# Performance work log

Measured on AMD Instinct MI355X. Metric: run time of the kernel, lower is better.

## Reference

```python
import jax, jax.numpy as jnp
import numpy as np
from math import log

MODEL_DIM = 512
NUM_HEADS = 8
DIM_HEAD = 64
INNER = NUM_HEADS * DIM_HEAD
B, L = 8, 1024
EPS = 1e-5


def setup_inputs() -> dict:
    key = jax.random.key(0)
    ks = jax.random.split(key, 9)
    x = jax.random.normal(ks[0], (B, L, MODEL_DIM), dtype=jnp.float32)
    gamma = jnp.ones((MODEL_DIM,), jnp.float32)
    beta = jnp.zeros((MODEL_DIM,), jnp.float32)
    w_qkv = jax.random.normal(ks[1], (3 * INNER, MODEL_DIM), jnp.float32) * (MODEL_DIM ** -0.5)
    b_qkv = jnp.zeros((3 * INNER,), jnp.float32)
    w_pos = jax.random.normal(ks[2], (INNER, MODEL_DIM), jnp.float32) * (MODEL_DIM ** -0.5)
    w_out = jax.random.normal(ks[3], (MODEL_DIM, INNER), jnp.float32) * (INNER ** -0.5)
    b_out = jnp.zeros((MODEL_DIM,), jnp.float32)
    # xavier_uniform for (num_heads, dim_head)
    bound = (6.0 / (NUM_HEADS + DIM_HEAD)) ** 0.5
    u_bias = jax.random.uniform(ks[4], (NUM_HEADS, DIM_HEAD), jnp.float32, -bound, bound)
    v_bias = jax.random.uniform(ks[5], (NUM_HEADS, DIM_HEAD), jnp.float32, -bound, bound)
    return {"x": x, "gamma": gamma, "beta": beta, "w_qkv": w_qkv, "b_qkv": b_qkv,
            "w_pos": w_pos, "w_out": w_out, "b_out": b_out, "u_bias": u_bias, "v_bias": v_bias}


def _rel_pos_emb(seq_len, d):
    # (L, D): (i - j) scaled by sinusoid frequencies, then cos on even cols, sin on odd cols
    rel = (jnp.arange(seq_len, dtype=jnp.float32)[:, None]
           - jnp.arange(d, dtype=jnp.float32)[None, :])
    freqs = jnp.exp(-jnp.arange(0, 2 * d, 2, dtype=jnp.float32) * (log(10000.0) / MODEL_DIM))
    angle = rel * freqs[None, :]
    even = (jnp.arange(d) % 2) == 0
    return jnp.where(even[None, :], jnp.cos(angle), jnp.sin(angle))  # (L, D)


def reference(x, gamma, beta, w_qkv, b_qkv, w_pos, w_out, b_out, u_bias, v_bias):
    b, l, d = x.shape
    h, dh = NUM_HEADS, DIM_HEAD
    # LayerNorm
    mu = jnp.mean(x, axis=-1, keepdims=True)
    var = jnp.mean(jnp.square(x - mu), axis=-1, keepdims=True)
    xn = (x - mu) * jax.lax.rsqrt(var + EPS) * gamma + beta
    # relative position embedding, identical per batch element
    pe = _rel_pos_emb(l, d)                      # (L, D)
    pos = (pe @ w_pos.T).reshape(l, h, dh)       # (L, H, Dh)
    pos = jnp.transpose(pos, (1, 0, 2))          # (H, L, Dh)
    # qkv
    qkv = xn @ w_qkv.T + b_qkv                   # (B, L, 3*inner)
    q, k, v = jnp.split(qkv, 3, axis=-1)
    def to_heads(t):
        return jnp.transpose(t.reshape(b, l, h, dh), (0, 2, 1, 3))  # (B,H,L,Dh)
    q, k, v = to_heads(q), to_heads(k), to_heads(v)
    scale = dh ** -0.5
    content = jnp.einsum('bhld,bhmd->bhlm', q + u_bias[None, :, None, :], k)
    pos_score = jnp.einsum('bhld,hmd->bhlm', q + v_bias[None, :, None, :], pos)
    attn = jax.nn.softmax((content + pos_score) * scale, axis=-1)
    out = jnp.einsum('bhlm,bhmd->bhld', attn, v)
    out = jnp.transpose(out, (0, 2, 1, 3)).reshape(b, l, h * dh)
    return out @ w_out.T + b_out  # dropout p=0.0 -> identity
```

## Files before the change

kernel.cpp:

```cpp
#include <hip/hip_runtime.h>
#include <math.h>

static constexpr int Bn = 8, Ln = 1024, Dm = 512, Hn = 8, DhN = 64;

typedef short bf16x8 __attribute__((ext_vector_type(8)));
typedef float f32x4 __attribute__((ext_vector_type(4)));
typedef _Float16 f16x4 __attribute__((ext_vector_type(4)));
typedef _Float16 f16x8 __attribute__((ext_vector_type(8)));
typedef unsigned int u32x4 __attribute__((ext_vector_type(4)));

#define QSCALE 0.1803368801111137f

static __device__ __forceinline__ unsigned short f2b(float f) {
  union { float f; unsigned int u; } x;
  x.f = f;
  unsigned int u = x.u;
  unsigned int r = (u + 0x7FFFu + ((u >> 16) & 1u)) >> 16;
  return (unsigned short)r;
}
static __device__ __forceinline__ float b2f(unsigned short u) {
  union { unsigned int u; float f; } x;
  x.u = ((unsigned int)u) << 16;
  return x.f;
}

#define GLDS16(g, l)                                                        \
  __builtin_amdgcn_global_load_lds((const __attribute__((address_space(1))) void*)(g), \
                                   (__attribute__((address_space(3))) void*)(l), 16, 0, 0)

__global__ __launch_bounds__(256) void prep1(const float* __restrict__ x,
                                             const float* __restrict__ gamma,
                                             const float* __restrict__ beta,
                                             unsigned short* __restrict__ xn,
                                             unsigned short* __restrict__ pe,
                                             const float* __restrict__ wq, unsigned short* __restrict__ wqb,
                                             const float* __restrict__ wp, unsigned short* __restrict__ wpb,
                                             const float* __restrict__ wo, unsigned short* __restrict__ wob) {
  int b = blockIdx.x;
  int t = threadIdx.x;
  if (b < 8192) {
    const float2 v = *(const float2*)(x + (size_t)b * Dm + t * 2);
    float s = v.x + v.y;
    float sq = v.x * v.x + v.y * v.y;
#pragma unroll
    for (int off = 32; off > 0; off >>= 1) {
      s += __shfl_down(s, off);
      sq += __shfl_down(sq, off);
    }
    __shared__ float red[8];
    int wave = t >> 6, lane = t & 63;
    if (lane == 0) { red[wave * 2] = s; red[wave * 2 + 1] = sq; }
    __syncthreads();
    float S = red[0] + red[2] + red[4] + red[6];
    float SQ = red[1] + red[3] + red[5] + red[7];
    float mu = S * (1.0f / Dm);
    float var = SQ * (1.0f / Dm) - mu * mu;
    float rstd = rsqrtf(var + 1e-5f);
    int c = t * 2;
    ushort2 o;
    o.x = f2b((v.x - mu) * rstd * gamma[c] + beta[c]);
    o.y = f2b((v.y - mu) * rstd * gamma[c + 1] + beta[c + 1]);
    *(ushort2*)(xn + (size_t)b * Dm + c) = o;
  } else if (b < 10240) {
    int idx = (b - 8192) * 256 + t;
    int l = idx >> 9, k = idx & 511;
    float freq = expf(-0.0359778921f * (float)k);
    float angle = (float)(l - k) * freq;
    pe[idx] = f2b((k & 1) ? sinf(angle) : cosf(angle));
  } else {
    int cb = b - 10240;
    const float* src;
    unsigned short* dst;
    int off;
    if (cb < 768) { src = wq; dst = wqb; off = cb; }
    else if (cb < 1024) { src = wp; dst = wpb; off = cb - 768; }
    else { src = wo; dst = wob; off = cb - 1024; }
    int i = off * 256 + t;
    float4 v = *(const float4*)(src + (size_t)i * 4);
    ushort4 o;
    o.x = f2b(v.x); o.y = f2b(v.y); o.z = f2b(v.z); o.w = f2b(v.w);
    *(ushort4*)(dst + (size_t)i * 4) = o;
  }
}

__global__ __launch_bounds__(256, 8) void gemm_mfma(const unsigned short* __restrict__ Ain,
                                                    const unsigned short* __restrict__ Bwin,
                                                    const float* __restrict__ biasin,
                                                    float* __restrict__ outfin,
                                                    unsigned short* __restrict__ oq,
                                                    unsigned short* __restrict__ ok,
                                                    unsigned short* __restrict__ ov,
                                                    const unsigned short* __restrict__ A2,
                                                    const unsigned short* __restrict__ B2,
                                                    float* __restrict__ outf2,
                                                    int K, int mode) {
  int by = blockIdx.y, bx = blockIdx.x;
  const unsigned short* A = Ain;
  const unsigned short* Bw = Bwin;
  const float* bias = biasin;
  float* outf = outfin;
  if (by >= 128) {
    if (bx >= 8) return;
    A = A2; Bw = B2; bias = nullptr; outf = outf2; mode = 1; by -= 128;
  }
  __shared__ alignas(16) unsigned short As[64 * 64];
  __shared__ alignas(16) unsigned short Bs[64 * 64];
  const int t = threadIdx.x;
  const int lane = t & 63, w = t >> 6;
  const int c = lane & 15, q8 = lane >> 4;
  const int wm = (w & 1) * 32, wn = (w >> 1) * 32;
  const int m0 = by * 64, n0 = bx * 64;

  f32x4 acc[2][2];
#pragma unroll
  for (int i = 0; i < 2; ++i)
#pragma unroll
    for (int j = 0; j < 2; ++j) acc[i][j] = (f32x4){0.f, 0.f, 0.f, 0.f};

  const int srow = lane >> 3;
  const int sgr = (lane & 7) ^ srow;

  for (int k0 = 0; k0 < K; k0 += 64) {
    __syncthreads();
#pragma unroll
    for (int j = 0; j < 2; ++j) {
      int r = j * 32 + w * 8 + srow;
      GLDS16(A + (size_t)(m0 + r) * K + k0 + sgr * 8, As + (j * 256 + w * 64 + lane) * 8);
      GLDS16(Bw + (size_t)(n0 + r) * K + k0 + sgr * 8, Bs + (j * 256 + w * 64 + lane) * 8);
    }
    __syncthreads();
#pragma unroll
    for (int kk = 0; kk < 2; ++kk) {
      bf16x8 a[2], b[2];
      const int q = kk * 4 + q8;
#pragma unroll
      for (int i = 0; i < 2; ++i) {
        int r = wm + i * 16 + c;
        a[i] = *(const bf16x8*)&As[(r * 8 + (q ^ (r & 7))) * 8];
      }
#pragma unroll
      for (int j = 0; j < 2; ++j) {
        int r = wn + j * 16 + c;
        b[j] = *(const bf16x8*)&Bs[(r * 8 + (q ^ (r & 7))) * 8];
      }
#pragma unroll
      for (int i = 0; i < 2; ++i)
#pragma unroll
        for (int j = 0; j < 2; ++j)
          acc[i][j] = __builtin_amdgcn_mfma_f32_16x16x32_bf16(a[i], b[j], acc[i][j], 0, 0, 0);
    }
  }
#pragma unroll
  for (int i = 0; i < 2; ++i) {
#pragma unroll
    for (int r = 0; r < 4; ++r) {
      int m = m0 + wm + i * 16 + q8 * 4 + r;
#pragma unroll
      for (int j = 0; j < 2; ++j) {
        int n = n0 + wn + j * 16 + c;
        float val = acc[i][j][r] + (bias ? bias[n] : 0.0f);
        if (mode == 0) {
          int part = n >> 9, h = (n >> 6) & 7, dh = n & 63;
          int bb = m >> 10, l = m & 1023;
          size_t idx = (size_t)((bb * 8 + h) * 1024 + l) * 64 + dh;
          if (part == 0) {
            oq[idx] = f2b(val * QSCALE);
          } else if (part == 1) {
            ok[idx] = f2b(val);
          } else {
            union { _Float16 h; unsigned short u; } cv;
            cv.h = (_Float16)val;
            ov[idx] = cv.u;
          }
        } else if (mode == 1) {
          int h = n >> 6, dh = n & 63;
          outf[(size_t)(h * 1024 + m) * 64 + dh] = val;
        } else {
          outf[(size_t)m * 512 + n] = val;
        }
      }
    }
  }
}

__global__ __launch_bounds__(256) void prep2(unsigned short* __restrict__ kbuf,
                                             const float* __restrict__ pos,
                                             const float* __restrict__ ub,
                                             const float* __restrict__ vbb,
                                             float* __restrict__ biasout,
                                             const unsigned short* __restrict__ v,
                                             unsigned short* __restrict__ vt) {
  int b = blockIdx.x;
  int t = threadIdx.x;
  if (b < 16384) {
    int wave = t >> 6, lane = t & 63;
    int g = b * 4 + wave;
    int h = (g >> 10) & 7;
    int m = g & 1023;
    float kv = b2f(kbuf[(size_t)g * 64 + lane]);
    float pv = pos[(size_t)(h * 1024 + m) * 64 + lane];
    float val = ub[h * 64 + lane] * kv + vbb[h * 64 + lane] * pv;
#pragma unroll
    for (int off = 32; off > 0; off >>= 1) val += __shfl_down(val, off);
    if (lane == 0) biasout[g] = val * QSCALE;
    kbuf[(size_t)g * 64 + lane] = f2b(kv + pv);
  } else {
    __shared__ unsigned short Ts[64 * 68];
    int bb = b - 16384;
    int bh = bb >> 4, lt = bb & 15;
    const unsigned short* vg = v + (size_t)bh * 65536 + lt * 4096;
#pragma unroll
    for (int s = 0; s < 4; ++s) {
      int idx = t + s * 256;
      int r = idx >> 4, c4 = (idx & 15) << 2;
      *(ushort4*)&Ts[r * 68 + c4] = *(const ushort4*)(vg + r * 64 + c4);
    }
    __syncthreads();
#pragma unroll
    for (int s = 0; s < 4; ++s) {
      int idx = t + s * 256;
      int d = idx >> 4, l4 = (idx & 15) << 2;
      ushort4 o;
      o.x = Ts[(l4 + 0) * 68 + d];
      o.y = Ts[(l4 + 1) * 68 + d];
      o.z = Ts[(l4 + 2) * 68 + d];
      o.w = Ts[(l4 + 3) * 68 + d];
      int pb = ((l4 >> 2) & 3) * 16 + ((l4 >> 4) & 3) * 4;
      *(ushort4*)(vt + (size_t)bh * 65536 + d * 1024 + lt * 64 + pb) = o;
    }
  }
}

__global__ __launch_bounds__(512) void flash_mfma(const unsigned short* __restrict__ qbf,
                                                  const unsigned short* __restrict__ kbf,
                                                  const unsigned short* __restrict__ vt,
                                                  const float* __restrict__ bias,
                                                  unsigned short* __restrict__ attn_out) {
  __shared__ alignas(16) unsigned short Ks[2][64 * 64];
  __shared__ alignas(16) unsigned short Vs[2][64 * 64];
  __shared__ alignas(16) float Bls[1024];
  const int t = threadIdx.x;
  const int lane = t & 63, w = t >> 6;
  const int c = lane & 15, q8 = lane >> 4;
  const int cc7 = c & 7;
  const int bh = blockIdx.y, qt = blockIdx.x;
  const unsigned short* qg = qbf + (size_t)bh * 65536;
  const unsigned short* kg = kbf + (size_t)bh * 65536;
  const unsigned short* vg = vt + (size_t)bh * 65536;
  const float* bg = bias + (size_t)bh * 1024;

  if (t < 256) GLDS16(bg + t * 4, Bls + t * 4);

  const int ql = qt * 128 + w * 16 + c;
  const bf16x8 bq0 = *(const bf16x8*)(qg + (size_t)ql * 64 + q8 * 8);
  const bf16x8 bq1 = *(const bf16x8*)(qg + (size_t)ql * 64 + 32 + q8 * 8);

  float m_st = -INFINITY, l_st = 0.0f;
  f32x4 o[4];
#pragma unroll
  for (int i = 0; i < 4; ++i) o[i] = (f32x4){0.f, 0.f, 0.f, 0.f};

  const int srow = lane >> 3;
  const int sgr = (lane & 7) ^ srow;
  const int r0 = w * 8 + srow;

  u32x4 pk[2], pv[2];
#pragma unroll
  for (int h = 0; h < 2; ++h) {
    pk[h] = *(const u32x4*)(kg + (size_t)(h * 64 + r0) * 64 + sgr * 8);
    pv[h] = *(const u32x4*)(vg + (size_t)r0 * 1024 + h * 64 + sgr * 8);
  }

  for (int it = 0; it < 8; ++it) {
    __syncthreads();
#pragma unroll
    for (int h = 0; h < 2; ++h) {
      *(u32x4*)&Ks[h][(r0 * 8 + (lane & 7)) * 8] = pk[h];
      *(u32x4*)&Vs[h][(r0 * 8 + (lane & 7)) * 8] = pv[h];
    }
    __syncthreads();
    if (it < 7) {
#pragma unroll
      for (int h = 0; h < 2; ++h) {
        pk[h] = *(const u32x4*)(kg + (size_t)((it + 1) * 128 + h * 64 + r0) * 64 + sgr * 8);
        pv[h] = *(const u32x4*)(vg + (size_t)r0 * 1024 + (it + 1) * 128 + h * 64 + sgr * 8);
      }
    }

    f32x4 sc[2][4];
#pragma unroll
    for (int h = 0; h < 2; ++h) {
#pragma unroll
      for (int nt = 0; nt < 4; ++nt) {
        f32x4 ci = *(const f32x4*)&Bls[it * 128 + h * 64 + nt * 16 + q8 * 4];
        const int row = nt * 16 + c;
        bf16x8 ak0 = *(const bf16x8*)&Ks[h][(row * 8 + (q8 ^ cc7)) * 8];
        bf16x8 ak1 = *(const bf16x8*)&Ks[h][(row * 8 + ((q8 + 4) ^ cc7)) * 8];
        ci = __builtin_amdgcn_mfma_f32_16x16x32_bf16(ak0, bq0, ci, 0, 0, 0);
        sc[h][nt] = __builtin_amdgcn_mfma_f32_16x16x32_bf16(ak1, bq1, ci, 0, 0, 0);
      }
    }
    float mx = sc[0][0][0];
#pragma unroll
    for (int h = 0; h < 2; ++h)
#pragma unroll
      for (int nt = 0; nt < 4; ++nt)
#pragma unroll
        for (int r = 0; r < 4; ++r) mx = fmaxf(mx, sc[h][nt][r]);
    mx = fmaxf(mx, __shfl_xor(mx, 16));
    mx = fmaxf(mx, __shfl_xor(mx, 32));
    float mn = fmaxf(m_st, mx);
    float al = __builtin_amdgcn_exp2f(m_st - mn);
    float su = 0.0f;
    f16x4 pf[2][4];
#pragma unroll
    for (int h = 0; h < 2; ++h)
#pragma unroll
      for (int nt = 0; nt < 4; ++nt)
#pragma unroll
        for (int r = 0; r < 4; ++r) {
          float p = __builtin_amdgcn_exp2f(sc[h][nt][r] - mn);
          su += p;
          pf[h][nt][r] = (_Float16)p;
        }
    su += __shfl_xor(su, 16);
    su += __shfl_xor(su, 32);
    l_st = l_st * al + su;
    m_st = mn;
#pragma unroll
    for (int i = 0; i < 4; ++i) o[i] *= al;
#pragma unroll
    for (int i = 0; i < 4; ++i) {
      const int row = i * 16 + c;
#pragma unroll
      for (int h = 0; h < 2; ++h) {
        f16x8 v01 = *(const f16x8*)&Vs[h][(row * 8 + ((2 * q8) ^ cc7)) * 8];
        f16x8 v23 = *(const f16x8*)&Vs[h][(row * 8 + ((2 * q8 + 1) ^ cc7)) * 8];
        f16x4 a0 = {v01[0], v01[1], v01[2], v01[3]};
        f16x4 a1 = {v01[4], v01[5], v01[6], v01[7]};
        f16x4 a2 = {v23[0], v23[1], v23[2], v23[3]};
        f16x4 a3 = {v23[4], v23[5], v23[6], v23[7]};
        o[i] = __builtin_amdgcn_mfma_f32_16x16x16f16(a0, pf[h][0], o[i], 0, 0, 0);
        o[i] = __builtin_amdgcn_mfma_f32_16x16x16f16(a1, pf[h][1], o[i], 0, 0, 0);
        o[i] = __builtin_amdgcn_mfma_f32_16x16x16f16(a2, pf[h][2], o[i], 0, 0, 0);
        o[i] = __builtin_amdgcn_mfma_f32_16x16x16f16(a3, pf[h][3], o[i], 0, 0, 0);
      }
    }
  }
  const int bidx = bh >> 3, h = bh & 7;
  float inv = 1.0f / l_st;
  size_t base = (size_t)(bidx * 1024 + ql) * 512 + h * 64;
#pragma unroll
  for (int i = 0; i < 4; ++i) {
    ushort4 ov4;
    ov4.x = f2b(o[i][0] * inv);
    ov4.y = f2b(o[i][1] * inv);
    ov4.z = f2b(o[i][2] * inv);
    ov4.w = f2b(o[i][3] * inv);
    *(ushort4*)(attn_out + base + i * 16 + q8 * 4) = ov4;
  }
}

extern "C" void kernel_launch(void* const* d_in, const int* in_sizes, int n_in,
                              void* d_out, int out_size, void* d_ws, size_t ws_size,
                              hipStream_t stream) {
  const float* x      = (const float*)d_in[0];
  const float* gamma  = (const float*)d_in[1];
  const float* beta   = (const float*)d_in[2];
  const float* w_qkv  = (const float*)d_in[3];
  const float* b_qkv  = (const float*)d_in[4];
  const float* w_pos  = (const float*)d_in[5];
  const float* w_out  = (const float*)d_in[6];
  const float* b_out  = (const float*)d_in[7];
  const float* u_bias = (const float*)d_in[8];
  const float* v_bias = (const float*)d_in[9];
  float* out = (float*)d_out;

  unsigned short* wsu = (unsigned short*)d_ws;
  unsigned short* xnb   = wsu;
  unsigned short* peb   = wsu + 4194304;
  unsigned short* wqkvb = wsu + 4718592;
  unsigned short* wposb = wsu + 5505024;
  unsigned short* woutb = wsu + 5767168;
  unsigned short* qbf   = wsu + 6291456;
  unsigned short* kbf   = wsu + 10485760;
  unsigned short* vbf   = wsu + 14680064;
  unsigned short* vtb   = wsu + 18874368;
  unsigned short* attnb = wsu + 23068672;
  float* posb  = (float*)(wsu + 27262976);
  float* biasb = (float*)(wsu + 28311552);

  prep1<<<11520, 256, 0, stream>>>(x, gamma, beta, xnb, peb,
                                   w_qkv, wqkvb, w_pos, wposb, w_out, woutb);
  gemm_mfma<<<dim3(24, 144), 256, 0, stream>>>(xnb, wqkvb, b_qkv, nullptr, qbf, kbf, vbf,
                                               peb, wposb, posb, 512, 0);
  prep2<<<17408, 256, 0, stream>>>(kbf, posb, u_bias, v_bias, biasb, vbf, vtb);
  flash_mfma<<<dim3(8, 64), 512, 0, stream>>>(qbf, kbf, vtb, biasb, attnb);
  gemm_mfma<<<dim3(8, 128), 256, 0, stream>>>(attnb, woutb, b_out, out, nullptr, nullptr, nullptr,
                                              nullptr, nullptr, nullptr, 512, 2);
}
```

Baseline: 177.8 us.

## Process two query tiles per wave in flash attention with 256-thread blocks

The flash attention kernel now runs 4 waves per block instead of 8, and each wave handles two 16-row query groups. Each K/V fragment read from shared memory therefore feeds twice as many MFMAs, and each thread loads twice as many K/V rows into LDS. The aim is to cut LDS read traffic and barrier cost per unit of work. In exchange, register pressure roughly doubles for accumulators and scores, and each block has fewer waves for latency hiding, partly offset by launch_bounds(256,2).

New measurement: 176.8 us. No clear change (-0.6%).

```diff
diff --git a/kernel.cpp b/kernel.cpp
--- a/kernel.cpp
+++ b/kernel.cpp
@@ -231,11 +231,11 @@
   }
 }
 
-__global__ __launch_bounds__(512) void flash_mfma(const unsigned short* __restrict__ qbf,
-                                                  const unsigned short* __restrict__ kbf,
-                                                  const unsigned short* __restrict__ vt,
-                                                  const float* __restrict__ bias,
-                                                  unsigned short* __restrict__ attn_out) {
+__global__ __launch_bounds__(256, 2) void flash_mfma(const unsigned short* __restrict__ qbf,
+                                                     const unsigned short* __restrict__ kbf,
+                                                     const unsigned short* __restrict__ vt,
+                                                     const float* __restrict__ bias,
+                                                     unsigned short* __restrict__ attn_out) {
   __shared__ alignas(16) unsigned short Ks[2][64 * 64];
   __shared__ alignas(16) unsigned short Vs[2][64 * 64];
   __shared__ alignas(16) float Bls[1024];
@@ -249,45 +249,60 @@
   const unsigned short* vg = vt + (size_t)bh * 65536;
   const float* bg = bias + (size_t)bh * 1024;
 
-  if (t < 256) GLDS16(bg + t * 4, Bls + t * 4);
-
-  const int ql = qt * 128 + w * 16 + c;
-  const bf16x8 bq0 = *(const bf16x8*)(qg + (size_t)ql * 64 + q8 * 8);
-  const bf16x8 bq1 = *(const bf16x8*)(qg + (size_t)ql * 64 + 32 + q8 * 8);
-
-  float m_st = -INFINITY, l_st = 0.0f;
-  f32x4 o[4];
-#pragma unroll
-  for (int i = 0; i < 4; ++i) o[i] = (f32x4){0.f, 0.f, 0.f, 0.f};
+  GLDS16(bg + t * 4, Bls + t * 4);
+
+  bf16x8 bq[2][2];
+#pragma unroll
+  for (int g = 0; g < 2; ++g) {
+    int qlg = qt * 128 + g * 64 + w * 16 + c;
+    bq[g][0] = *(const bf16x8*)(qg + (size_t)qlg * 64 + q8 * 8);
+    bq[g][1] = *(const bf16x8*)(qg + (size_t)qlg * 64 + 32 + q8 * 8);
+  }
+
+  float m_st[2] = {-INFINITY, -INFINITY}, l_st[2] = {0.0f, 0.0f};
+  f32x4 o[2][4];
+#pragma unroll
+  for (int g = 0; g < 2; ++g)
+#pragma unroll
+    for (int i = 0; i < 4; ++i) o[g][i] = (f32x4){0.f, 0.f, 0.f, 0.f};
 
   const int srow = lane >> 3;
   const int sgr = (lane & 7) ^ srow;
-  const int r0 = w * 8 + srow;
-
-  u32x4 pk[2], pv[2];
-#pragma unroll
-  for (int h = 0; h < 2; ++h) {
-    pk[h] = *(const u32x4*)(kg + (size_t)(h * 64 + r0) * 64 + sgr * 8);
-    pv[h] = *(const u32x4*)(vg + (size_t)r0 * 1024 + h * 64 + sgr * 8);
-  }
+  const int r0 = w * 16 + srow;
+
+  u32x4 pk[2][2], pv[2][2];
+#pragma unroll
+  for (int h = 0; h < 2; ++h)
+#pragma unroll
+    for (int j = 0; j < 2; ++j) {
+      int r = r0 + j * 8;
+      pk[h][j] = *(const u32x4*)(kg + (size_t)(h * 64 + r) * 64 + sgr * 8);
+      pv[h][j] = *(const u32x4*)(vg + (size_t)r * 1024 + h * 64 + sgr * 8);
+    }
 
   for (int it = 0; it < 8; ++it) {
     __syncthreads();
 #pragma unroll
-    for (int h = 0; h < 2; ++h) {
-      *(u32x4*)&Ks[h][(r0 * 8 + (lane & 7)) * 8] = pk[h];
-      *(u32x4*)&Vs[h][(r0 * 8 + (lane & 7)) * 8] = pv[h];
-    }
+    for (int h = 0; h < 2; ++h)
+#pragma unroll
+      for (int j = 0; j < 2; ++j) {
+        int r = r0 + j * 8;
+        *(u32x4*)&Ks[h][(r * 8 + (lane & 7)) * 8] = pk[h][j];
+        *(u32x4*)&Vs[h][(r * 8 + (lane & 7)) * 8] = pv[h][j];
+      }
     __syncthreads();
     if (it < 7) {
 #pragma unroll
-      for (int h = 0; h < 2; ++h) {
-        pk[h] = *(const u32x4*)(kg + (size_t)((it + 1) * 128 + h * 64 + r0) * 64 + sgr * 8);
-        pv[h] = *(const u32x4*)(vg + (size_t)r0 * 1024 + (it + 1) * 128 + h * 64 + sgr * 8);
-      }
-    }
-
-    f32x4 sc[2][4];
+      for (int h = 0; h < 2; ++h)
+#pragma unroll
+        for (int j = 0; j < 2; ++j) {
+          int r = r0 + j * 8;
+          pk[h][j] = *(const u32x4*)(kg + (size_t)((it + 1) * 128 + h * 64 + r) * 64 + sgr * 8);
+          pv[h][j] = *(const u32x4*)(vg + (size_t)r * 1024 + (it + 1) * 128 + h * 64 + sgr * 8);
+        }
+    }
+
+    f32x4 sc[2][2][4];
 #pragma unroll
     for (int h = 0; h < 2; ++h) {
 #pragma unroll
@@ -296,39 +311,45 @@
         const int row = nt * 16 + c;
         bf16x8 ak0 = *(const bf16x8*)&Ks[h][(row * 8 + (q8 ^ cc7)) * 8];
         bf16x8 ak1 = *(const bf16x8*)&Ks[h][(row * 8 + ((q8 + 4) ^ cc7)) * 8];
-        ci = __builtin_amdgcn_mfma_f32_16x16x32_bf16(ak0, bq0, ci, 0, 0, 0);
-        sc[h][nt] = __builtin_amdgcn_mfma_f32_16x16x32_bf16(ak1, bq1, ci, 0, 0, 0);
-      }
-    }
-    float mx = sc[0][0][0];
-#pragma unroll
-    for (int h = 0; h < 2; ++h)
-#pragma unroll
-      for (int nt = 0; nt < 4; ++nt)
-#pragma unroll
-        for (int r = 0; r < 4; ++r) mx = fmaxf(mx, sc[h][nt][r]);
-    mx = fmaxf(mx, __shfl_xor(mx, 16));
-    mx = fmaxf(mx, __shfl_xor(mx, 32));
-    float mn = fmaxf(m_st, mx);
-    float al = __builtin_amdgcn_exp2f(m_st - mn);
-    float su = 0.0f;
-    f16x4 pf[2][4];
-#pragma unroll
-    for (int h = 0; h < 2; ++h)
-#pragma unroll
-      for (int nt = 0; nt < 4; ++nt)
-#pragma unroll
-        for (int r = 0; r < 4; ++r) {
-          float p = __builtin_amdgcn_exp2f(sc[h][nt][r] - mn);
-          su += p;
-          pf[h][nt][r] = (_Float16)p;
+#pragma unroll
+        for (int g = 0; g < 2; ++g) {
+          f32x4 z = __builtin_amdgcn_mfma_f32_16x16x32_bf16(ak0, bq[g][0], ci, 0, 0, 0);
+          sc[g][h][nt] = __builtin_amdgcn_mfma_f32_16x16x32_bf16(ak1, bq[g][1], z, 0, 0, 0);
         }
-    su += __shfl_xor(su, 16);
-    su += __shfl_xor(su, 32);
-    l_st = l_st * al + su;
-    m_st = mn;
-#pragma unroll
-    for (int i = 0; i < 4; ++i) o[i] *= al;
+      }
+    }
+    f16x4 pf[2][2][4];
+#pragma unroll
+    for (int g = 0; g < 2; ++g) {
+      float mx = sc[g][0][0][0];
+#pragma unroll
+      for (int h = 0; h < 2; ++h)
+#pragma unroll
+        for (int nt = 0; nt < 4; ++nt)
+#pragma unroll
+          for (int r = 0; r < 4; ++r) mx = fmaxf(mx, sc[g][h][nt][r]);
+      mx = fmaxf(mx, __shfl_xor(mx, 16));
+      mx = fmaxf(mx, __shfl_xor(mx, 32));
+      float mn = fmaxf(m_st[g], mx);
+      float al = __builtin_amdgcn_exp2f(m_st[g] - mn);
+      float su = 0.0f;
+#pragma unroll
+      for (int h = 0; h < 2; ++h)
+#pragma unroll
+        for (int nt = 0; nt < 4; ++nt)
+#pragma unroll
+          for (int r = 0; r < 4; ++r) {
+            float p = __builtin_amdgcn_exp2f(sc[g][h][nt][r] - mn);
+            su += p;
+            pf[g][h][nt][r] = (_Float16)p;
+          }
+      su += __shfl_xor(su, 16);
+      su += __shfl_xor(su, 32);
+      l_st[g] = l_st[g] * al + su;
+      m_st[g] = mn;
+#pragma unroll
+      for (int i = 0; i < 4; ++i) o[g][i] *= al;
+    }
 #pragma unroll
     for (int i = 0; i < 4; ++i) {
       const int row = i * 16 + c;
@@ -340,24 +361,31 @@
         f16x4 a1 = {v01[4], v01[5], v01[6], v01[7]};
         f16x4 a2 = {v23[0], v23[1], v23[2], v23[3]};
         f16x4 a3 = {v23[4], v23[5], v23[6], v23[7]};
-        o[i] = __builtin_amdgcn_mfma_f32_16x16x16f16(a0, pf[h][0], o[i], 0, 0, 0);
-        o[i] = __builtin_amdgcn_mfma_f32_16x16x16f16(a1, pf[h][1], o[i], 0, 0, 0);
-        o[i] = __builtin_amdgcn_mfma_f32_16x16x16f16(a2, pf[h][2], o[i], 0, 0, 0);
-        o[i] = __builtin_amdgcn_mfma_f32_16x16x16f16(a3, pf[h][3], o[i], 0, 0, 0);
+#pragma unroll
+        for (int g = 0; g < 2; ++g) {
+          o[g][i] = __builtin_amdgcn_mfma_f32_16x16x16f16(a0, pf[g][h][0], o[g][i], 0, 0, 0);
+          o[g][i] = __builtin_amdgcn_mfma_f32_16x16x16f16(a1, pf[g][h][1], o[g][i], 0, 0, 0);
+          o[g][i] = __builtin_amdgcn_mfma_f32_16x16x16f16(a2, pf[g][h][2], o[g][i], 0, 0, 0);
+          o[g][i] = __builtin_amdgcn_mfma_f32_16x16x16f16(a3, pf[g][h][3], o[g][i], 0, 0, 0);
+        }
       }
     }
   }
   const int bidx = bh >> 3, h = bh & 7;
-  float inv = 1.0f / l_st;
-  size_t base = (size_t)(bidx * 1024 + ql) * 512 + h * 64;
-#pragma unroll
-  for (int i = 0; i < 4; ++i) {
-    ushort4 ov4;
-    ov4.x = f2b(o[i][0] * inv);
-    ov4.y = f2b(o[i][1] * inv);
-    ov4.z = f2b(o[i][2] * inv);
-    ov4.w = f2b(o[i][3] * inv);
-    *(ushort4*)(attn_out + base + i * 16 + q8 * 4) = ov4;
+#pragma unroll
+  for (int g = 0; g < 2; ++g) {
+    int qlg = qt * 128 + g * 64 + w * 16 + c;
+    float inv = 1.0f / l_st[g];
+    size_t base = (size_t)(bidx * 1024 + qlg) * 512 + h * 64;
+#pragma unroll
+    for (int i = 0; i < 4; ++i) {
+      ushort4 ov4;
+      ov4.x = f2b(o[g][i][0] * inv);
+      ov4.y = f2b(o[g][i][1] * inv);
+      ov4.z = f2b(o[g][i][2] * inv);
+      ov4.w = f2b(o[g][i][3] * inv);
+      *(ushort4*)(attn_out + base + i * 16 + q8 * 4) = ov4;
+    }
   }
 }
 
@@ -395,7 +423,7 @@
   gemm_mfma<<<dim3(24, 144), 256, 0, stream>>>(xnb, wqkvb, b_qkv, nullptr, qbf, kbf, vbf,
                                                peb, wposb, posb, 512, 0);
   prep2<<<17408, 256, 0, stream>>>(kbf, posb, u_bias, v_bias, biasb, vbf, vtb);
-  flash_mfma<<<dim3(8, 64), 512, 0, stream>>>(qbf, kbf, vtb, biasb, attnb);
+  flash_mfma<<<dim3(8, 64), 256, 0, stream>>>(qbf, kbf, vtb, biasb, attnb);
   gemm_mfma<<<dim3(8, 128), 256, 0, stream>>>(attnb, woutb, b_out, out, nullptr, nullptr, nullptr,
                                               nullptr, nullptr, nullptr, 512, 2);
 }
```
